# Kernel tuning notes

Hardware: AMD Instinct MI355X
Metric: run time of the kernel (lower is better)

The kernel has to match this reference:

```python
import jax, jax.numpy as jnp
import numpy as np

D_MODEL = 768
NUM_HEADS = 12
D_K = D_MODEL // NUM_HEADS
SCALE = float(np.sqrt(D_K))


def setup_inputs() -> dict:
    key = jax.random.key(0)
    ks = jax.random.split(key, 9)
    B, S, D = 2, 2048, D_MODEL
    std = 1.0 / np.sqrt(D)
    x = jax.random.normal(ks[0], (B, S, D), dtype=jnp.float32)
    attention_mask = jnp.ones((B, S), dtype=jnp.int32)
    # Linear params: weight [out, in] (torch convention), bias [out]
    Wq = jax.random.normal(ks[1], (D, D), dtype=jnp.float32) * std
    bq = jax.random.normal(ks[2], (D,), dtype=jnp.float32) * 0.01
    Wk = jax.random.normal(ks[3], (D, D), dtype=jnp.float32) * std
    bk = jax.random.normal(ks[4], (D,), dtype=jnp.float32) * 0.01
    Wv = jax.random.normal(ks[5], (D, D), dtype=jnp.float32) * std
    bv = jax.random.normal(ks[6], (D,), dtype=jnp.float32) * 0.01
    Wo = jax.random.normal(ks[7], (D, D), dtype=jnp.float32) * std
    bo = jax.random.normal(ks[8], (D,), dtype=jnp.float32) * 0.01
    return {"x": x, "attention_mask": attention_mask,
            "Wq": Wq, "bq": bq, "Wk": Wk, "bk": bk,
            "Wv": Wv, "bv": bv, "Wo": Wo, "bo": bo}


def reference(x, attention_mask, Wq, bq, Wk, bk, Wv, bv, Wo, bo):
    B, S, D = x.shape
    H, Dk = NUM_HEADS, D_K
    # QKV projections (torch Linear: x @ W.T + b)
    q = (x @ Wq.T + bq).reshape(B, S, H, Dk).transpose(0, 2, 1, 3)  # [B,H,S,Dk]
    k = (x @ Wk.T + bk).reshape(B, S, H, Dk).transpose(0, 2, 1, 3)
    v = (x @ Wv.T + bv).reshape(B, S, H, Dk).transpose(0, 2, 1, 3)
    scores = jnp.einsum('bhqd,bhkd->bhqk', q, k) / SCALE  # [B,H,S,S]
    mask = attention_mask[:, None, None, :]  # [B,1,1,S]
    scores = jnp.where(mask == 0, jnp.float32(-jnp.inf), scores)
    attn = jax.nn.softmax(scores, axis=-1)
    # dropout is identity in eval mode
    ctx = jnp.einsum('bhqk,bhkd->bhqd', attn, v)  # [B,H,S,Dk]
    ctx = ctx.transpose(0, 2, 1, 3).reshape(B, S, D)
    return ctx @ Wo.T + bo
```

## Files before the change

### kernel.cpp

```cpp
#include <hip/hip_runtime.h>
#include <stdint.h>

#define NHEAD 12
#define DKH   64
#define BB    2
#define SS    2048
#define DMOD  768
#define MTOT  (BB*SS)
#define NCHUNK 2
#define CHS   (SS/NCHUNK)
#define QBLK  128
#define NT    (CHS/64)

typedef __attribute__((ext_vector_type(8)))  _Float16 half8;
typedef __attribute__((ext_vector_type(4)))  _Float16 half4;
typedef __attribute__((ext_vector_type(2)))  __fp16   fp16x2;
typedef __attribute__((ext_vector_type(4)))  float    f32x4;
typedef __attribute__((ext_vector_type(16))) float    f32x16;

typedef __attribute__((address_space(1))) const void gv_t;
typedef __attribute__((address_space(3))) void       lv_t;

__device__ inline float fexp2(float x) { return __builtin_amdgcn_exp2f(x); }
__device__ inline int pk2(float a, float b) {
    union { fp16x2 h; int i; } u;
    u.h = __builtin_amdgcn_cvt_pkrtz(a, b);
    return u.i;
}

__global__ void k_cvt(const float* __restrict__ in, _Float16* __restrict__ out, int n) {
    int i = (blockIdx.x * 256 + threadIdx.x) * 4;
    if (i >= n) return;
    float4 v = *(const float4*)(in + i);
    half4 o;
    o.x = (_Float16)v.x; o.y = (_Float16)v.y; o.z = (_Float16)v.z; o.w = (_Float16)v.w;
    *(half4*)(out + i) = o;
}

__global__ void k_cvtw(const float* __restrict__ w0, const float* __restrict__ w1,
                       const float* __restrict__ w2, const float* __restrict__ w3,
                       _Float16* __restrict__ o0, _Float16* __restrict__ o1,
                       _Float16* __restrict__ o2, _Float16* __restrict__ o3) {
    const float* in; _Float16* out;
    switch (blockIdx.y) {
        case 0: in = w0; out = o0; break;
        case 1: in = w1; out = o1; break;
        case 2: in = w2; out = o2; break;
        default: in = w3; out = o3; break;
    }
    int i = (blockIdx.x * 256 + threadIdx.x) * 4;
    float4 v = *(const float4*)(in + i);
    half4 o;
    o.x = (_Float16)v.x; o.y = (_Float16)v.y; o.z = (_Float16)v.z; o.w = (_Float16)v.w;
    *(half4*)(out + i) = o;
}

template<int MODE>
__global__ __launch_bounds__(256, 2) void k_gemm(
    const _Float16* __restrict__ A, const _Float16* __restrict__ Bm,
    const float* __restrict__ bias0, const float* __restrict__ bias1, const float* __restrict__ bias2,
    float* __restrict__ outF,
    _Float16* __restrict__ Qd, _Float16* __restrict__ Kd, _Float16* __restrict__ Vtd,
    int K, int Ncols)
{
    __shared__ _Float16 As[128 * 32];
    __shared__ _Float16 Bs[128 * 32];
    const int tid = threadIdx.x;
    const int w = tid >> 6, l = tid & 63, lr = l & 15, lg = l >> 4;
    const int bm = blockIdx.y * 128, bn = blockIdx.x * 128;
    const int wm = (w >> 1) * 64, wn = (w & 1) * 64;
    f32x4 acc[4][4] = {};

    for (int k0 = 0; k0 < K; k0 += 32) {
        __syncthreads();
#pragma unroll
        for (int i = 0; i < 2; ++i) {
            int o = w * 2048 + i * 1024 + l * 16;
            int row = o >> 6;
            int c8  = (o >> 4) & 3;
            __builtin_amdgcn_global_load_lds(
                (gv_t*)((const char*)A + ((size_t)(bm + row) * K + k0 + c8 * 8) * 2),
                (lv_t*)((char*)As + w * 2048 + i * 1024), 16, 0, 0);
            __builtin_amdgcn_global_load_lds(
                (gv_t*)((const char*)Bm + ((size_t)(bn + row) * K + k0 + c8 * 8) * 2),
                (lv_t*)((char*)Bs + w * 2048 + i * 1024), 16, 0, 0);
        }
        __syncthreads();
        half8 af[4], bf[4];
#pragma unroll
        for (int f = 0; f < 4; ++f) {
            af[f] = *(const half8*)((const char*)As + (wm + f * 16 + lr) * 64 + lg * 16);
            bf[f] = *(const half8*)((const char*)Bs + (wn + f * 16 + lr) * 64 + lg * 16);
        }
#pragma unroll
        for (int fm = 0; fm < 4; ++fm)
#pragma unroll
            for (int fn = 0; fn < 4; ++fn)
                acc[fm][fn] = __builtin_amdgcn_mfma_f32_16x16x32_f16(af[fm], bf[fn], acc[fm][fn], 0, 0, 0);
    }

#pragma unroll
    for (int fm = 0; fm < 4; ++fm) {
#pragma unroll
        for (int fn = 0; fn < 4; ++fn) {
            int n = bn + wn + fn * 16 + lr;
            if (MODE == 0) {
                float bia = bias0[n];
#pragma unroll
                for (int j = 0; j < 4; ++j) {
                    int m = bm + wm + fm * 16 + lg * 4 + j;
                    outF[(size_t)m * Ncols + n] = acc[fm][fn][j] + bia;
                }
            } else {
                int qkv = n / 768, nn = n - qkv * 768;
                const float* bp = (qkv == 0) ? bias0 : (qkv == 1 ? bias1 : bias2);
                float bia = bp[nn];
                int h = nn >> 6, dk = nn & 63;
                int m0 = bm + wm + fm * 16 + lg * 4;
                int b = m0 >> 11;
                int s0 = m0 & 2047;
                size_t head = (size_t)b * NHEAD + h;
                if (qkv == 2) {
                    half4 pk;
#pragma unroll
                    for (int j = 0; j < 4; ++j) pk[j] = (_Float16)(acc[fm][fn][j] + bia);
                    *(half4*)(Vtd + (head * DKH + dk) * SS + s0) = pk;
                } else {
                    _Float16* dst = (qkv == 0) ? Qd : Kd;
                    float qsc = (qkv == 0) ? 0.18033688011f : 1.0f;
#pragma unroll
                    for (int j = 0; j < 4; ++j)
                        dst[(head * SS + (s0 + j)) * DKH + dk] = (_Float16)((acc[fm][fn][j] + bia) * qsc);
                }
            }
        }
    }
}

__global__ __launch_bounds__(256, 3) void k_attn(
    const _Float16* __restrict__ Qd, const _Float16* __restrict__ Kd,
    const _Float16* __restrict__ Vtd, const int* __restrict__ mask,
    _Float16* __restrict__ Opart, float* __restrict__ Mpart, float* __restrict__ Lpart)
{
    __shared__ _Float16 Ks[2 * 64 * 64];
    __shared__ _Float16 Vs[2 * 64 * 64];
    const int tid = threadIdx.x, w = tid >> 6, l = tid & 63;
    const int lq = l & 31, lhi = l >> 5;
    const int head  = blockIdx.x;
    const int qt    = blockIdx.y;
    const int chunk = blockIdx.z;
    const int b = head / NHEAD;
    const char* Qh = (const char*)(Qd + (size_t)head * SS * DKH);
    const char* Kh = (const char*)(Kd + (size_t)head * SS * DKH) + (size_t)chunk * CHS * 128;
    const char* Vh = (const char*)(Vtd + (size_t)head * DKH * SS);
    const int vcb = chunk * CHS * 2;

    const int q = qt * QBLK + w * 32 + lq;
    half8 qf[4];
#pragma unroll
    for (int kd = 0; kd < 4; ++kd)
        qf[kd] = *(const half8*)(Qh + ((size_t)q * 64 + kd * 16 + lhi * 8) * 2);

    f32x16 accO[2] = {};
    float m = -__builtin_inff(), lsum = 0.f;

    auto STAGE = [&](int kt2, int buf) {
#pragma unroll
        for (int i = 0; i < 2; ++i) {
            int o  = w * 2048 + i * 1024 + l * 16;
            int lo = o ^ (((o >> 7) & 7) << 4);
            __builtin_amdgcn_global_load_lds(
                (gv_t*)(Kh + (size_t)kt2 * 8192 + lo),
                (lv_t*)((char*)Ks + buf * 8192 + w * 2048 + i * 1024), 16, 0, 0);
            int dv = lo >> 7, inner = lo & 127;
            __builtin_amdgcn_global_load_lds(
                (gv_t*)(Vh + (size_t)dv * 4096 + vcb + kt2 * 128 + inner),
                (lv_t*)((char*)Vs + buf * 8192 + w * 2048 + i * 1024), 16, 0, 0);
        }
    };

    STAGE(0, 0);
    int cur = 0;

    for (int kt = 0; kt < NT; ++kt) {
        __syncthreads();
        if (kt < NT - 1) STAGE(kt + 1, cur ^ 1);
        int mv = mask[b * SS + chunk * CHS + kt * 64 + l];
        unsigned long long bal = __ballot(mv != 0);
        const char* kb = (const char*)Ks + cur * 8192;
        const char* vb = (const char*)Vs + cur * 8192;

        f32x16 s0 = {}, s1 = {};
#pragma unroll
        for (int kd = 0; kd < 4; ++kd) {
            int col = kd * 32 + lhi * 16;
            int ob0 = (lq * 128 + col) ^ ((lq & 7) << 4);
            half8 kf0 = *(const half8*)(kb + ob0);
            s0 = __builtin_amdgcn_mfma_f32_32x32x16_f16(kf0, qf[kd], s0, 0, 0, 0);
            int ob1 = ((32 + lq) * 128 + col) ^ ((lq & 7) << 4);
            half8 kf1 = *(const half8*)(kb + ob1);
            s1 = __builtin_amdgcn_mfma_f32_32x32x16_f16(kf1, qf[kd], s1, 0, 0, 0);
        }

        if (bal != ~0ull) {
#pragma unroll
            for (int r = 0; r < 16; ++r) {
                int kv0 = (r & 3) + 8 * (r >> 2) + 4 * lhi;
                if (!((bal >> kv0) & 1))        s0[r] = -__builtin_inff();
                if (!((bal >> (kv0 + 32)) & 1)) s1[r] = -__builtin_inff();
            }
        }

        float t[16];
#pragma unroll
        for (int i = 0; i < 16; ++i) t[i] = fmaxf(s0[i], s1[i]);
#pragma unroll
        for (int i = 0; i < 8; ++i) t[i] = fmaxf(t[i], t[i + 8]);
#pragma unroll
        for (int i = 0; i < 4; ++i) t[i] = fmaxf(t[i], t[i + 4]);
        t[0] = fmaxf(fmaxf(t[0], t[2]), fmaxf(t[1], t[3]));
        float pmax = fmaxf(t[0], __shfl_xor(t[0], 32, 64));

        if (!__all(pmax <= m + 3.0f)) {
            float mnew = fmaxf(m, pmax);
            float f = fexp2(m - mnew);
            m = mnew; lsum *= f;
            accO[0] *= f; accO[1] *= f;
        }
        float mex = fmaxf(m, -1e30f);

#pragma unroll
        for (int i = 0; i < 16; ++i) { s0[i] = fexp2(s0[i] - mex); s1[i] = fexp2(s1[i] - mex); }
#pragma unroll
        for (int i = 0; i < 16; ++i) t[i] = s0[i] + s1[i];
#pragma unroll
        for (int i = 0; i < 8; ++i) t[i] = t[i] + t[i + 8];
#pragma unroll
        for (int i = 0; i < 4; ++i) t[i] = t[i] + t[i + 4];
        t[0] = (t[0] + t[2]) + (t[1] + t[3]);
        lsum += t[0] + __shfl_xor(t[0], 32, 64);

        union PF { int w[4]; half8 h; } pf[4];
        {
            int W[8];
#pragma unroll
            for (int mm = 0; mm < 8; ++mm) W[mm] = pk2(s0[2 * mm], s0[2 * mm + 1]);
            asm("v_permlane32_swap_b32 %0, %1" : "+v"(W[0]), "+v"(W[2]));
            asm("v_permlane32_swap_b32 %0, %1" : "+v"(W[1]), "+v"(W[3]));
            asm("v_permlane32_swap_b32 %0, %1" : "+v"(W[4]), "+v"(W[6]));
            asm("v_permlane32_swap_b32 %0, %1" : "+v"(W[5]), "+v"(W[7]));
            pf[0].w[0] = W[0]; pf[0].w[1] = W[1]; pf[0].w[2] = W[2]; pf[0].w[3] = W[3];
            pf[1].w[0] = W[4]; pf[1].w[1] = W[5]; pf[1].w[2] = W[6]; pf[1].w[3] = W[7];
#pragma unroll
            for (int mm = 0; mm < 8; ++mm) W[mm] = pk2(s1[2 * mm], s1[2 * mm + 1]);
            asm("v_permlane32_swap_b32 %0, %1" : "+v"(W[0]), "+v"(W[2]));
            asm("v_permlane32_swap_b32 %0, %1" : "+v"(W[1]), "+v"(W[3]));
            asm("v_permlane32_swap_b32 %0, %1" : "+v"(W[4]), "+v"(W[6]));
            asm("v_permlane32_swap_b32 %0, %1" : "+v"(W[5]), "+v"(W[7]));
            pf[2].w[0] = W[0]; pf[2].w[1] = W[1]; pf[2].w[2] = W[2]; pf[2].w[3] = W[3];
            pf[3].w[0] = W[4]; pf[3].w[1] = W[5]; pf[3].w[2] = W[6]; pf[3].w[3] = W[7];
        }

#pragma unroll
        for (int cc = 0; cc < 4; ++cc) {
            int col = cc * 32 + lhi * 16;
#pragma unroll
            for (int ds = 0; ds < 2; ++ds) {
                int vrow = ds * 32 + lq;
                int ob = (vrow * 128 + col) ^ ((lq & 7) << 4);
                half8 vf = *(const half8*)(vb + ob);
                accO[ds] = __builtin_amdgcn_mfma_f32_32x32x16_f16(vf, pf[cc].h, accO[ds], 0, 0, 0);
            }
        }
        cur ^= 1;
    }

    const size_t prow = (size_t)(chunk * BB * NHEAD + head) * SS;
    if (lhi == 0) { Mpart[prow + q] = m; Lpart[prow + q] = lsum; }
#pragma unroll
    for (int ds = 0; ds < 2; ++ds)
#pragma unroll
        for (int rq = 0; rq < 4; ++rq) {
            half4 hv;
#pragma unroll
            for (int j = 0; j < 4; ++j) hv[j] = (_Float16)accO[ds][rq * 4 + j];
            *(half4*)(Opart + (prow + q) * DKH + ds * 32 + rq * 8 + lhi * 4) = hv;
        }
}

__global__ __launch_bounds__(256) void k_merge(
    const _Float16* __restrict__ Opart, const float* __restrict__ Mpart,
    const float* __restrict__ Lpart, _Float16* __restrict__ Ctx)
{
    int row  = blockIdx.x * 4 + (threadIdx.x >> 6);
    int lane = threadIdx.x & 63;
    int head = row >> 11, q = row & 2047;
    int b = head / NHEAD, h = head - b * NHEAD;
    float m[NCHUNK], lv[NCHUNK], M = -__builtin_inff();
#pragma unroll
    for (int c = 0; c < NCHUNK; ++c) {
        size_t pr = (size_t)(c * BB * NHEAD + head) * SS + q;
        m[c] = Mpart[pr]; lv[c] = Lpart[pr];
        M = fmaxf(M, m[c]);
    }
    float outv = 0.f;
    if (M > -1e37f) {
        float L = 0.f, acc = 0.f;
#pragma unroll
        for (int c = 0; c < NCHUNK; ++c) {
            float wgt = fexp2(m[c] - M);
            L += lv[c] * wgt;
            acc += wgt * (float)Opart[((size_t)(c * BB * NHEAD + head) * SS + q) * DKH + lane];
        }
        outv = acc / L;
    }
    Ctx[((size_t)(b * SS) + q) * DMOD + h * DKH + lane] = (_Float16)outv;
}

extern "C" void kernel_launch(void* const* d_in, const int* in_sizes, int n_in,
                              void* d_out, int out_size, void* d_ws, size_t ws_size,
                              hipStream_t stream) {
    const float* x  = (const float*)d_in[0];
    const int*  msk = (const int*)d_in[1];
    const float* Wq = (const float*)d_in[2];
    const float* bq = (const float*)d_in[3];
    const float* Wk = (const float*)d_in[4];
    const float* bk = (const float*)d_in[5];
    const float* Wv = (const float*)d_in[6];
    const float* bv = (const float*)d_in[7];
    const float* Wo = (const float*)d_in[8];
    const float* bo = (const float*)d_in[9];

    char* ws = (char*)d_ws;
    _Float16* Xb   = (_Float16*)(ws);
    _Float16* Wqkv = (_Float16*)(ws + 6291456);
    _Float16* Wob  = (_Float16*)(ws + 9830400);
    _Float16* Qd   = (_Float16*)(ws + 11010048);
    _Float16* Kd   = (_Float16*)(ws + 17301504);
    _Float16* Vtd  = (_Float16*)(ws + 23592960);
    _Float16* Ctxb = (_Float16*)(ws + 29884416);
    _Float16* Opart= (_Float16*)(ws + 36175872);
    float*    Mpart= (float*)   (ws + 48758784);
    float*    Lpart= (float*)   (ws + 49152000);

    k_cvt<<<3072, 256, 0, stream>>>(x, Xb, MTOT * DMOD);
    k_cvtw<<<dim3(576, 4), 256, 0, stream>>>(Wq, Wk, Wv, Wo,
                                             Wqkv, Wqkv + 589824, Wqkv + 1179648, Wob);

    k_gemm<1><<<dim3(18, 32), 256, 0, stream>>>(Xb, Wqkv, bq, bk, bv,
                                                nullptr, Qd, Kd, Vtd, DMOD, 0);
    k_attn<<<dim3(24, SS / QBLK, NCHUNK), 256, 0, stream>>>(Qd, Kd, Vtd, msk, Opart, Mpart, Lpart);
    k_merge<<<12288, 256, 0, stream>>>(Opart, Mpart, Lpart, Ctxb);
    k_gemm<0><<<dim3(6, 32), 256, 0, stream>>>(Ctxb, Wob, bo, nullptr, nullptr,
                                               (float*)d_out, nullptr, nullptr, nullptr,
                                               DMOD, DMOD);
}
```

Baseline: 115.5 us.

## Double GEMM K-tile to 64 with XOR-swizzled LDS and fuse conversion kernels

```diff
diff --git a/kernel.cpp b/kernel.cpp
--- a/kernel.cpp
+++ b/kernel.cpp
@@ -28,27 +28,20 @@
     return u.i;
 }
 
-__global__ void k_cvt(const float* __restrict__ in, _Float16* __restrict__ out, int n) {
-    int i = (blockIdx.x * 256 + threadIdx.x) * 4;
-    if (i >= n) return;
-    float4 v = *(const float4*)(in + i);
-    half4 o;
-    o.x = (_Float16)v.x; o.y = (_Float16)v.y; o.z = (_Float16)v.z; o.w = (_Float16)v.w;
-    *(half4*)(out + i) = o;
-}
-
-__global__ void k_cvtw(const float* __restrict__ w0, const float* __restrict__ w1,
-                       const float* __restrict__ w2, const float* __restrict__ w3,
-                       _Float16* __restrict__ o0, _Float16* __restrict__ o1,
-                       _Float16* __restrict__ o2, _Float16* __restrict__ o3) {
-    const float* in; _Float16* out;
-    switch (blockIdx.y) {
-        case 0: in = w0; out = o0; break;
-        case 1: in = w1; out = o1; break;
-        case 2: in = w2; out = o2; break;
-        default: in = w3; out = o3; break;
-    }
-    int i = (blockIdx.x * 256 + threadIdx.x) * 4;
+__global__ void k_cvtall(const float* __restrict__ x,
+                         const float* __restrict__ w0, const float* __restrict__ w1,
+                         const float* __restrict__ w2, const float* __restrict__ w3,
+                         _Float16* __restrict__ xb,
+                         _Float16* __restrict__ o0, _Float16* __restrict__ o1,
+                         _Float16* __restrict__ o2, _Float16* __restrict__ o3) {
+    const float* in; _Float16* out; int base;
+    int blk = blockIdx.x;
+    if (blk < 3072)      { in = x;  out = xb; base = blk; }
+    else if (blk < 3648) { in = w0; out = o0; base = blk - 3072; }
+    else if (blk < 4224) { in = w1; out = o1; base = blk - 3648; }
+    else if (blk < 4800) { in = w2; out = o2; base = blk - 4224; }
+    else                 { in = w3; out = o3; base = blk - 4800; }
+    int i = (base * 256 + threadIdx.x) * 4;
     float4 v = *(const float4*)(in + i);
     half4 o;
     o.x = (_Float16)v.x; o.y = (_Float16)v.y; o.z = (_Float16)v.z; o.w = (_Float16)v.w;
@@ -63,40 +56,48 @@
     _Float16* __restrict__ Qd, _Float16* __restrict__ Kd, _Float16* __restrict__ Vtd,
     int K, int Ncols)
 {
-    __shared__ _Float16 As[128 * 32];
-    __shared__ _Float16 Bs[128 * 32];
+    __shared__ _Float16 As[128 * 64];
+    __shared__ _Float16 Bs[128 * 64];
     const int tid = threadIdx.x;
     const int w = tid >> 6, l = tid & 63, lr = l & 15, lg = l >> 4;
     const int bm = blockIdx.y * 128, bn = blockIdx.x * 128;
     const int wm = (w >> 1) * 64, wn = (w & 1) * 64;
     f32x4 acc[4][4] = {};
 
-    for (int k0 = 0; k0 < K; k0 += 32) {
+    for (int k0 = 0; k0 < K; k0 += 64) {
         __syncthreads();
 #pragma unroll
-        for (int i = 0; i < 2; ++i) {
-            int o = w * 2048 + i * 1024 + l * 16;
-            int row = o >> 6;
-            int c8  = (o >> 4) & 3;
+        for (int i = 0; i < 4; ++i) {
+            int o  = w * 4096 + i * 1024 + l * 16;
+            int lo = o ^ (((o >> 7) & 7) << 4);
+            int row = lo >> 7;
+            int colb = lo & 127;
             __builtin_amdgcn_global_load_lds(
-                (gv_t*)((const char*)A + ((size_t)(bm + row) * K + k0 + c8 * 8) * 2),
-                (lv_t*)((char*)As + w * 2048 + i * 1024), 16, 0, 0);
+                (gv_t*)((const char*)A + ((size_t)(bm + row) * K + k0) * 2 + colb),
+                (lv_t*)((char*)As + w * 4096 + i * 1024), 16, 0, 0);
             __builtin_amdgcn_global_load_lds(
-                (gv_t*)((const char*)Bm + ((size_t)(bn + row) * K + k0 + c8 * 8) * 2),
-                (lv_t*)((char*)Bs + w * 2048 + i * 1024), 16, 0, 0);
+                (gv_t*)((const char*)Bm + ((size_t)(bn + row) * K + k0) * 2 + colb),
+                (lv_t*)((char*)Bs + w * 4096 + i * 1024), 16, 0, 0);
         }
         __syncthreads();
-        half8 af[4], bf[4];
-#pragma unroll
-        for (int f = 0; f < 4; ++f) {
-            af[f] = *(const half8*)((const char*)As + (wm + f * 16 + lr) * 64 + lg * 16);
-            bf[f] = *(const half8*)((const char*)Bs + (wn + f * 16 + lr) * 64 + lg * 16);
-        }
-#pragma unroll
-        for (int fm = 0; fm < 4; ++fm)
-#pragma unroll
-            for (int fn = 0; fn < 4; ++fn)
-                acc[fm][fn] = __builtin_amdgcn_mfma_f32_16x16x32_f16(af[fm], bf[fn], acc[fm][fn], 0, 0, 0);
+#pragma unroll
+        for (int kk = 0; kk < 2; ++kk) {
+            half8 af[4], bf[4];
+#pragma unroll
+            for (int f = 0; f < 4; ++f) {
+                int ob = ((wm + f * 16 + lr) * 128 + kk * 64 + lg * 16) ^ ((lr & 7) << 4);
+                af[f] = *(const half8*)((const char*)As + ob);
+                int ob2 = ((wn + f * 16 + lr) * 128 + kk * 64 + lg * 16) ^ ((lr & 7) << 4);
+                bf[f] = *(const half8*)((const char*)Bs + ob2);
+            }
+            __builtin_amdgcn_s_setprio(1);
+#pragma unroll
+            for (int fm = 0; fm < 4; ++fm)
+#pragma unroll
+                for (int fn = 0; fn < 4; ++fn)
+                    acc[fm][fn] = __builtin_amdgcn_mfma_f32_16x16x32_f16(af[fm], bf[fn], acc[fm][fn], 0, 0, 0);
+            __builtin_amdgcn_s_setprio(0);
+        }
     }
 
 #pragma unroll
@@ -343,13 +344,12 @@
     float*    Mpart= (float*)   (ws + 48758784);
     float*    Lpart= (float*)   (ws + 49152000);
 
-    k_cvt<<<3072, 256, 0, stream>>>(x, Xb, MTOT * DMOD);
-    k_cvtw<<<dim3(576, 4), 256, 0, stream>>>(Wq, Wk, Wv, Wo,
-                                             Wqkv, Wqkv + 589824, Wqkv + 1179648, Wob);
+    k_cvtall<<<5376, 256, 0, stream>>>(x, Wq, Wk, Wv, Wo,
+                                       Xb, Wqkv, Wqkv + 589824, Wqkv + 1179648, Wob);
 
     k_gemm<1><<<dim3(18, 32), 256, 0, stream>>>(Xb, Wqkv, bq, bk, bv,
                                                 nullptr, Qd, Kd, Vtd, DMOD, 0);
-    k_attn<<<dim3(24, SS / QBLK, NCHUNK), 256, 0, stream>>>(Qd, Kd, Vtd, msk, Opart, Mpart, Lpart);
+    k_attn<<<dim3(24, 16, NCHUNK), 256, 0, stream>>>(Qd, Kd, Vtd, msk, Opart, Mpart, Lpart);
     k_merge<<<12288, 256, 0, stream>>>(Opart, Mpart, Lpart, Ctxb);
     k_gemm<0><<<dim3(6, 32), 256, 0, stream>>>(Ctxb, Wob, bo, nullptr, nullptr,
                                                (float*)d_out, nullptr, nullptr, nullptr,
```

After: 106.0 us. 8.2% less time.
